# Performance work log

Measured on AMD Instinct MI355X. Metric: run time of the kernel, lower is better.

## Reference

```python
import jax, jax.numpy as jnp
import numpy as np
from jax import lax

EPS = 1e-5
SLOPE = 0.2

def knn_idx(x, k):
    # x: [B, C, N] -> neighbor indices [B, N, k] (largest negative sq-dist, self included)
    inner = jnp.einsum('bcn,bcm->bnm', x, x)          # [B,N,N]
    xx = jnp.sum(x * x, axis=1)                        # [B,N]
    pair = 2.0 * inner - xx[:, :, None] - xx[:, None, :]
    return lax.top_k(pair, k)[1]                       # [B,N,k]

def graph_feature(x, idx):
    # x: [B,C,N], idx: [B,N,k] -> edge features [B,N,k,2C] = (x_j - x_i, x_i)
    feat = jnp.transpose(x, (0, 2, 1))                 # [B,N,C]
    nbr = jax.vmap(lambda f, i: f[i])(feat, idx)       # [B,N,k,C]
    ctr = jnp.broadcast_to(feat[:, :, None, :], nbr.shape)
    return jnp.concatenate([nbr - ctr, ctr], axis=-1)  # [B,N,k,2C]

def bn(x, gamma, beta, axes):
    mu = jnp.mean(x, axis=axes, keepdims=True)
    var = jnp.var(x, axis=axes, keepdims=True)
    return (x - mu) * lax.rsqrt(var + EPS) * gamma + beta

def edge_conv(e, w, gamma, beta):
    # e: [B,N,k,2C], w: [O,2C] (1x1 conv, no bias) -> [B,N,O] after BN+LeakyReLU+max over k
    h = jnp.einsum('bnkc,oc->bnko', e, w)
    h = jax.nn.leaky_relu(bn(h, gamma, beta, (0, 1, 2)), SLOPE)
    return jnp.max(h, axis=2)                          # [B,N,O]

def setup_inputs() -> dict:
    key = jax.random.key(0)
    ks = jax.random.split(key, 8)
    B, C, N, O = 8, 3, 4096, 64
    x = jax.random.normal(ks[0], (B, C, N), jnp.float32)
    w_s = jax.random.normal(ks[1], (O, 2 * C), jnp.float32) * (1.0 / np.sqrt(2 * C))
    w_l = jax.random.normal(ks[2], (O, 2 * C), jnp.float32) * (1.0 / np.sqrt(2 * C))
    w_f = jax.random.normal(ks[3], (O, 2 * O), jnp.float32) * (1.0 / np.sqrt(2 * O))
    g_s = jnp.ones((O,)); b_s = jnp.zeros((O,))
    g_l = jnp.ones((O,)); b_l = jnp.zeros((O,))
    g_f = jnp.ones((O,)); b_f = jnp.zeros((O,))
    return {"x": x, "w_s": w_s, "g_s": g_s, "b_s": b_s,
            "w_l": w_l, "g_l": g_l, "b_l": b_l,
            "w_f": w_f, "g_f": g_f, "b_f": b_f}

def reference(x, w_s, g_s, b_s, w_l, g_l, b_l, w_f, g_f, b_f):
    K_SMALL, K_LARGE = 20, 40
    idx_s = knn_idx(x, K_SMALL)
    idx_l = knn_idx(x, K_LARGE)
    h_s = edge_conv(graph_feature(x, idx_s), w_s, g_s, b_s)   # [B,N,O]
    h_l = edge_conv(graph_feature(x, idx_l), w_l, g_l, b_l)   # [B,N,O]
    h = jnp.concatenate([h_s, h_l], axis=-1)                  # [B,N,2O]
    h = jnp.einsum('bnc,oc->bno', h, w_f)                     # fuse 1x1 conv
    h = jax.nn.leaky_relu(bn(h, g_f, b_f, (0, 1)), SLOPE)
    return jnp.transpose(h, (0, 2, 1))                        # [B,O,N]
```

## Files before the change

### kernel.cpp

```cpp
#include <hip/hip_runtime.h>

#define B_ 8
#define N_ 4096
#define O_ 64
#define KL 40
#define KS 20
#define EPSV 1e-5
#define SLOPE 0.2f

typedef unsigned long long u64;
typedef unsigned int u32;

__device__ __forceinline__ float leaky(float v) { return v >= 0.f ? v : SLOPE * v; }

__device__ __forceinline__ u32 mfloat(float x) {
    const u32 u = __float_as_uint(x);
    return (u & 0x80000000u) ? ~u : (u | 0x80000000u);
}
__device__ __forceinline__ float unmfloat(u32 m) {
    return __uint_as_float((m & 0x80000000u) ? (m ^ 0x80000000u) : ~m);
}

template <int S>
__device__ __forceinline__ u64 xor_ex64(u64 v, int dsaddr) {
    if constexpr (S == 1 || S == 2 || S == 8) {
        constexpr int CTRL = (S == 1) ? 0xB1 : (S == 2) ? 0x4E : 0x128;
        const int lo = __builtin_amdgcn_update_dpp(0, (int)(u32)v, CTRL, 0xF, 0xF, true);
        const int hi = __builtin_amdgcn_update_dpp(0, (int)(u32)(v >> 32), CTRL, 0xF, 0xF, true);
        return ((u64)(u32)hi << 32) | (u32)lo;
    } else {
        const int lo = __builtin_amdgcn_ds_bpermute(dsaddr, (int)(u32)v);
        const int hi = __builtin_amdgcn_ds_bpermute(dsaddr, (int)(u32)(v >> 32));
        return ((u64)(u32)hi << 32) | (u32)lo;
    }
}

template <int K, int S>
__device__ __forceinline__ void stage_pair(u64& a, u64& e, int lane, int dsaddr) {
    const u64 oa = xor_ex64<S>(a, dsaddr);
    const u64 oe = xor_ex64<S>(e, dsaddr);
    const bool sel = (((lane & K) == 0) == ((lane & S) == 0));
    a = ((a < oa) == sel) ? a : oa;
    e = ((e < oe) == sel) ? e : oe;
}

__device__ __forceinline__ void sort64_pair(u64& a, u64& e, int lane,
                                            int a4, int a16, int a32) {
    stage_pair<2, 1>(a, e, lane, 0);
    stage_pair<4, 2>(a, e, lane, 0);    stage_pair<4, 1>(a, e, lane, 0);
    stage_pair<8, 4>(a, e, lane, a4);   stage_pair<8, 2>(a, e, lane, 0);    stage_pair<8, 1>(a, e, lane, 0);
    stage_pair<16, 8>(a, e, lane, 0);   stage_pair<16, 4>(a, e, lane, a4);  stage_pair<16, 2>(a, e, lane, 0);   stage_pair<16, 1>(a, e, lane, 0);
    stage_pair<32, 16>(a, e, lane, a16); stage_pair<32, 8>(a, e, lane, 0);  stage_pair<32, 4>(a, e, lane, a4);  stage_pair<32, 2>(a, e, lane, 0);  stage_pair<32, 1>(a, e, lane, 0);
    stage_pair<64, 32>(a, e, lane, a32); stage_pair<64, 16>(a, e, lane, a16); stage_pair<64, 8>(a, e, lane, 0); stage_pair<64, 4>(a, e, lane, a4); stage_pair<64, 2>(a, e, lane, 0); stage_pair<64, 1>(a, e, lane, 0);
}

__device__ __forceinline__ void merge_pair(u64& L0, u64& L1, u64 a, u64 e, int lane,
                                           int a4, int a16, int a32, int a63) {
    const u64 ra = xor_ex64<63>(a, a63);
    const u64 re = xor_ex64<63>(e, a63);
    L0 = (L0 < ra) ? L0 : ra;
    L1 = (L1 < re) ? L1 : re;
    stage_pair<0, 32>(L0, L1, lane, a32);
    stage_pair<0, 16>(L0, L1, lane, a16);
    stage_pair<0, 8>(L0, L1, lane, 0);
    stage_pair<0, 4>(L0, L1, lane, a4);
    stage_pair<0, 2>(L0, L1, lane, 0);
    stage_pair<0, 1>(L0, L1, lane, 0);
}

__global__ __launch_bounds__(1024) void bucket_kernel(const float* __restrict__ x,
                                                      float4* __restrict__ sxp,
                                                      int* __restrict__ perm,
                                                      float2* __restrict__ cb) {
    __shared__ int hist[256];
    __shared__ int ofs[256];
    __shared__ u32 xsm[4096];
    __shared__ float redmin[16], redmax[16];
    __shared__ u32 wmin[64], wmax[64];
    const int b = blockIdx.x;
    const float* xb = x + (size_t)b * 3 * N_;
    const int t = threadIdx.x;
    float xv[4];
    float mn = INFINITY, mx = -INFINITY;
#pragma unroll
    for (int p = 0; p < 4; ++p) {
        xv[p] = xb[t + p * 1024];
        mn = fminf(mn, xv[p]); mx = fmaxf(mx, xv[p]);
    }
#pragma unroll
    for (int s = 1; s < 64; s <<= 1) {
        mn = fminf(mn, __shfl_xor(mn, s));
        mx = fmaxf(mx, __shfl_xor(mx, s));
    }
    if ((t & 63) == 0) { redmin[t >> 6] = mn; redmax[t >> 6] = mx; }
    if (t < 256) hist[t] = 0;
    __syncthreads();
    if (t == 0) {
        float m0 = INFINITY, m1 = -INFINITY;
        for (int w = 0; w < 16; ++w) { m0 = fminf(m0, redmin[w]); m1 = fmaxf(m1, redmax[w]); }
        redmin[0] = m0; redmax[0] = m1;
    }
    __syncthreads();
    const float xmin = redmin[0];
    const float scale = 256.0f / fmaxf(redmax[0] - xmin, 1e-20f);
    int bk[4];
#pragma unroll
    for (int p = 0; p < 4; ++p) {
        bk[p] = min(255, max(0, (int)((xv[p] - xmin) * scale)));
        atomicAdd(&hist[bk[p]], 1);
    }
    __syncthreads();
    if (t == 0) {
        int acc = 0;
        for (int k = 0; k < 256; ++k) { ofs[k] = acc; acc += hist[k]; }
    }
    if (t < 64) { wmin[t] = 0xFFFFFFFFu; wmax[t] = 0; }
    __syncthreads();
#pragma unroll
    for (int p = 0; p < 4; ++p) {
        const int i = t + p * 1024;
        const int dst = atomicAdd(&ofs[bk[p]], 1);
        const float cx = xv[p], cy = xb[N_ + i], cz = xb[2 * N_ + i];
        sxp[((size_t)b << 12) + dst] = make_float4(2.f * cx, 2.f * cy, 2.f * cz,
                                                   -(cx * cx + cy * cy + cz * cz));
        perm[(b << 12) + dst] = i;
        xsm[dst] = mfloat(cx);
    }
    __syncthreads();
#pragma unroll
    for (int p = 0; p < 4; ++p) {
        const int pos = t + p * 1024;
        const int w = pos >> 6;
        atomicMin(&wmin[w], xsm[pos]);
        atomicMax(&wmax[w], xsm[pos]);
    }
    __syncthreads();
    if (t == 0) {
        u32 sm = 0xFFFFFFFFu;
        for (int w = 63; w >= 0; --w) { sm = min(sm, wmin[w]); wmin[w] = sm; }
        u32 pm = 0;
        for (int w = 0; w < 64; ++w) { pm = max(pm, wmax[w]); wmax[w] = pm; }
    }
    __syncthreads();
    if (t < 64) cb[(b << 6) + t] = make_float2(unmfloat(wmin[t]), unmfloat(wmax[t]));
}

__global__ __launch_bounds__(256, 8) void knn_kernel(const float4* __restrict__ sxp,
                                                     const int* __restrict__ perm,
                                                     const float2* __restrict__ cb,
                                                     const float* __restrict__ w_s,
                                                     const float* __restrict__ w_l,
                                                     int* __restrict__ idx_out,
                                                     float* __restrict__ A_s,
                                                     float* __restrict__ C_s,
                                                     float* __restrict__ A_l,
                                                     float* __restrict__ C_l) {
    __shared__ u64 buf[4][2][128];
    __shared__ float2 cbl[64];
    const int sbid = ((blockIdx.x & 7) << 9) | (blockIdx.x >> 3);
    const int b = sbid >> 9;
    const int qbase = (sbid & 511) << 3;
    const int tid = threadIdx.x;
    const int wave = tid >> 6, lane = tid & 63;
    if (tid < 64) cbl[tid] = cb[(b << 6) + tid];
    const int a4 = (lane ^ 4) << 2, a16 = (lane ^ 16) << 2;
    const int a32 = (lane ^ 32) << 2, a63 = (lane ^ 63) << 2;
    const float4* sp = sxp + ((size_t)b << 12);
    const int* pm = perm + (b << 12);
    const int i0 = qbase + wave * 2;
    const float4 p0 = sp[i0], p1 = sp[i0 + 1];
    const float qx0 = 0.5f * p0.x, qy0 = 0.5f * p0.y, qz0 = 0.5f * p0.z, nw0 = p0.w;
    const float qx1 = 0.5f * p1.x, qy1 = 0.5f * p1.y, qz1 = 0.5f * p1.z, nw1 = p1.w;
    const float qxmin = fminf(qx0, qx1), qxmax = fmaxf(qx0, qx1);
    u64 L0 = ~0ull, L1 = ~0ull;
    float th0 = -INFINITY, th1 = -INFINITY;
    int cnt0 = 0, cnt1 = 0;
    __syncthreads();
    const int home = i0 >> 6;
    int cl = home - 1, cr = home + 1;
    bool openL = (cl >= 0), openR = (cr < 64);
    bool takeR = true;
    int c = home;
    for (;;) {
        {
            const int js = (c << 6) + lane;
            const float4 cd = sp[js];
            const float d0 = fmaf(qx0, cd.x, fmaf(qy0, cd.y, fmaf(qz0, cd.z, cd.w + nw0)));
            const float d1 = fmaf(qx1, cd.x, fmaf(qy1, cd.y, fmaf(qz1, cd.z, cd.w + nw1)));
            const bool pr0 = (d0 >= th0), pr1 = (d1 >= th1);
            const u64 m0 = __ballot(pr0), m1 = __ballot(pr1);
            if (m0) {
                const int pos = cnt0 + __builtin_amdgcn_mbcnt_hi(
                    (u32)(m0 >> 32), __builtin_amdgcn_mbcnt_lo((u32)m0, 0));
                if (pr0) {
                    const u32 kd = __float_as_uint(fminf(d0, -0.0f));
                    buf[wave][0][pos] = ((u64)kd << 32) | (u32)pm[js];
                }
                cnt0 += __popcll(m0);
            }
            if (m1) {
                const int pos = cnt1 + __builtin_amdgcn_mbcnt_hi(
                    (u32)(m1 >> 32), __builtin_amdgcn_mbcnt_lo((u32)m1, 0));
                if (pr1) {
                    const u32 kd = __float_as_uint(fminf(d1, -0.0f));
                    buf[wave][1][pos] = ((u64)kd << 32) | (u32)pm[js];
                }
                cnt1 += __popcll(m1);
            }
            if ((cnt0 | cnt1) >= 64) {
                const int t0 = min(cnt0, 64), t1 = min(cnt1, 64);
                u64 a = (lane < t0) ? buf[wave][0][cnt0 - t0 + lane] : ~0ull;
                u64 e = (lane < t1) ? buf[wave][1][cnt1 - t1 + lane] : ~0ull;
                sort64_pair(a, e, lane, a4, a16, a32);
                merge_pair(L0, L1, a, e, lane, a4, a16, a32, a63);
                th0 = __uint_as_float((u32)__builtin_amdgcn_readlane((int)(u32)(L0 >> 32), KL - 1));
                th1 = __uint_as_float((u32)__builtin_amdgcn_readlane((int)(u32)(L1 >> 32), KL - 1));
                cnt0 -= t0; cnt1 -= t1;
            }
        }
        bool done = false;
        for (;;) {
            if (!openL && !openR) { done = true; break; }
            const bool pickR = openR && (takeR || !openL);
            takeR = !pickR;
            const float r2 = -fminf(th0, th1);
            if (pickR) {
                const float dx = cbl[cr].x - qxmax;
                if (dx > 0.f && dx * dx > r2) { openR = false; continue; }
                c = cr++;
                if (cr >= 64) openR = false;
                break;
            } else {
                const float dx = qxmin - cbl[cl].y;
                if (dx > 0.f && dx * dx > r2) { openL = false; continue; }
                c = cl--;
                if (cl < 0) openL = false;
                break;
            }
        }
        if (done) break;
    }
    if ((cnt0 | cnt1) > 0) {
        u64 a = (lane < cnt0) ? buf[wave][0][lane] : ~0ull;
        u64 e = (lane < cnt1) ? buf[wave][1][lane] : ~0ull;
        sort64_pair(a, e, lane, a4, a16, a32);
        merge_pair(L0, L1, a, e, lane, a4, a16, a32, a63);
    }
    const int oi0 = pm[i0], oi1 = pm[i0 + 1];
    if (lane < KL) {
        idx_out[(size_t)((b << 12) + oi0) * KL + lane] = (int)(u32)L0;
        idx_out[(size_t)((b << 12) + oi1) * KL + lane] = (int)(u32)L1;
    }
    for (int t2 = tid; t2 < 8 * 64; t2 += 256) {
        const int s = qbase + (t2 >> 6), o = t2 & 63;
        const float4 pp = sp[s];
        const float px = 0.5f * pp.x, py = 0.5f * pp.y, pz = 0.5f * pp.z;
        const int io = pm[s];
        const float* ws6 = w_s + o * 6;
        const float* wl6 = w_l + o * 6;
        const size_t gid = (size_t)((b << 12) + io) * 64 + o;
        A_s[gid] = ws6[0] * px + ws6[1] * py + ws6[2] * pz;
        C_s[gid] = (ws6[3] - ws6[0]) * px + (ws6[4] - ws6[1]) * py + (ws6[5] - ws6[2]) * pz;
        A_l[gid] = wl6[0] * px + wl6[1] * py + wl6[2] * pz;
        C_l[gid] = (wl6[3] - wl6[0]) * px + (wl6[4] - wl6[1]) * py + (wl6[5] - wl6[2]) * pz;
    }
}

__global__ __launch_bounds__(256) void gather_kernel(const int* __restrict__ idx,
    const float* __restrict__ A_s, const float* __restrict__ C_s,
    const float* __restrict__ A_l, const float* __restrict__ C_l,
    float* __restrict__ max_s, float* __restrict__ min_s,
    float* __restrict__ max_l, float* __restrict__ min_l,
    float* __restrict__ partial1) {
    const int tid = threadIdx.x;
    const int wave = tid >> 6, lane = tid & 63;
    const int sbid = ((blockIdx.x & 7) << 10) + (blockIdx.x >> 3);
    const int bn = sbid * 4 + wave;
    const int b = bn >> 12;
    const int jb = b << 12;
    const int* ip = idx + (size_t)bn * KL;
    const float cs = C_s[(size_t)bn * 64 + lane];
    const float cl = C_l[(size_t)bn * 64 + lane];
    float mxs = -INFINITY, mns = INFINITY, mxl = -INFINITY, mnl = INFINITY;
    float sums = 0.f, sss = 0.f, suml = 0.f, ssl = 0.f;
#pragma unroll
    for (int k = 0; k < KL; ++k) {
        const int j = ip[k];
        const float hl = A_l[(size_t)(jb + j) * 64 + lane] + cl;
        mxl = fmaxf(mxl, hl); mnl = fminf(mnl, hl);
        suml += hl; ssl = fmaf(hl, hl, ssl);
        if (k < KS) {
            const float hs = A_s[(size_t)(jb + j) * 64 + lane] + cs;
            mxs = fmaxf(mxs, hs); mns = fminf(mns, hs);
            sums += hs; sss = fmaf(hs, hs, sss);
        }
    }
    max_s[(size_t)bn * 64 + lane] = mxs; min_s[(size_t)bn * 64 + lane] = mns;
    max_l[(size_t)bn * 64 + lane] = mxl; min_l[(size_t)bn * 64 + lane] = mnl;
    __shared__ float red[4][4][64];
    red[0][wave][lane] = sums; red[1][wave][lane] = sss;
    red[2][wave][lane] = suml; red[3][wave][lane] = ssl;
    __syncthreads();
    const int st = tid >> 6;
    const int o = tid & 63;
    partial1[(size_t)blockIdx.x * 256 + tid] =
        red[st][0][o] + red[st][1][o] + red[st][2][o] + red[st][3][o];
}

__global__ void reduce1a_kernel(const float* __restrict__ partial1, double* __restrict__ partialD1) {
    const int t = threadIdx.x;
    double acc = 0.0;
    const int r0 = blockIdx.x * 64;
    for (int r = 0; r < 64; ++r) acc += (double)partial1[(size_t)(r0 + r) * 256 + t];
    partialD1[(size_t)blockIdx.x * 256 + t] = acc;
}

__global__ void reduce1b_kernel(const double* __restrict__ partialD1,
                                const float* __restrict__ g_s, const float* __restrict__ b_s,
                                const float* __restrict__ g_l, const float* __restrict__ b_l,
                                float* __restrict__ sb1) {
    const int t = threadIdx.x;
    double acc = 0.0;
    for (int r = 0; r < 128; ++r) acc += partialD1[(size_t)r * 256 + t];
    __shared__ double sums[256];
    sums[t] = acc;
    __syncthreads();
    if (t < 64) {
        const double ns = (double)B_ * N_ * KS;
        const double nl = (double)B_ * N_ * KL;
        double mu = sums[t] / ns;
        double var = sums[64 + t] / ns - mu * mu;
        double sc = (double)g_s[t] / sqrt(var + EPSV);
        sb1[t] = (float)sc;
        sb1[64 + t] = (float)((double)b_s[t] - mu * sc);
        mu = sums[128 + t] / nl;
        var = sums[192 + t] / nl - mu * mu;
        sc = (double)g_l[t] / sqrt(var + EPSV);
        sb1[128 + t] = (float)sc;
        sb1[192 + t] = (float)((double)b_l[t] - mu * sc);
    }
}

__global__ __launch_bounds__(256) void fuse_kernel(
    const float* __restrict__ max_s, const float* __restrict__ min_s,
    const float* __restrict__ max_l, const float* __restrict__ min_l,
    const float* __restrict__ sb1, const float* __restrict__ w_f,
    float* __restrict__ f_buf, float* __restrict__ partial2) {
    __shared__ float wfT[128 * 64];
    __shared__ float av[4][128];
    __shared__ float red[2][4][64];
    const int tid = threadIdx.x;
    for (int t = tid; t < 8192; t += 256) {
        const int c = t >> 6, o = t & 63;
        wfT[t] = w_f[o * 128 + c];
    }
    const int sbid = ((blockIdx.x & 7) << 8) + (blockIdx.x >> 3);
    const int wave = tid >> 6, lane = tid & 63;
    const float sc_s = sb1[lane], bi_s = sb1[64 + lane];
    const float sc_l = sb1[128 + lane], bi_l = sb1[192 + lane];
    float sum_f = 0.f, ss_f = 0.f;
    __syncthreads();
    for (int p = 0; p < 4; ++p) {
        const int bn = (sbid * 4 + wave) * 4 + p;
        const size_t base = (size_t)bn * 64 + lane;
        const float hs = sc_s >= 0.f ? max_s[base] : min_s[base];
        const float a_s = leaky(fmaf(sc_s, hs, bi_s));
        const float hl = sc_l >= 0.f ? max_l[base] : min_l[base];
        const float a_l = leaky(fmaf(sc_l, hl, bi_l));
        av[wave][lane] = a_s;
        av[wave][64 + lane] = a_l;
        float acc = 0.f;
#pragma unroll
        for (int c = 0; c < 128; ++c) acc = fmaf(wfT[c * 64 + lane], av[wave][c], acc);
        f_buf[base] = acc;
        sum_f += acc;
        ss_f = fmaf(acc, acc, ss_f);
    }
    red[0][wave][lane] = sum_f;
    red[1][wave][lane] = ss_f;
    __syncthreads();
    if (tid < 128) {
        const int st = tid >> 6, o = tid & 63;
        partial2[(size_t)blockIdx.x * 128 + tid] =
            red[st][0][o] + red[st][1][o] + red[st][2][o] + red[st][3][o];
    }
}

__global__ void reduce2a_kernel(const float* __restrict__ partial2, double* __restrict__ partialD2) {
    const int t = threadIdx.x;
    double acc = 0.0;
    const int r0 = blockIdx.x * 32;
    for (int r = 0; r < 32; ++r) acc += (double)partial2[(size_t)(r0 + r) * 128 + t];
    partialD2[(size_t)blockIdx.x * 128 + t] = acc;
}

__global__ void reduce2b_kernel(const double* __restrict__ partialD2,
                                const float* __restrict__ g_f, const float* __restrict__ b_f,
                                float* __restrict__ sb2) {
    const int t = threadIdx.x;
    double acc = 0.0;
    for (int r = 0; r < 64; ++r) acc += partialD2[(size_t)r * 128 + t];
    __shared__ double sums[128];
    sums[t] = acc;
    __syncthreads();
    if (t < 64) {
        const double n = (double)B_ * N_;
        const double mu = sums[t] / n;
        const double var = sums[64 + t] / n - mu * mu;
        const double sc = (double)g_f[t] / sqrt(var + EPSV);
        sb2[t] = (float)sc;
        sb2[64 + t] = (float)((double)b_f[t] - mu * sc);
    }
}

__global__ __launch_bounds__(256) void final_kernel(const float* __restrict__ f_buf,
                                                    const float* __restrict__ sb2,
                                                    float* __restrict__ out) {
    __shared__ float tile[64][65];
    const int sbid = ((blockIdx.x & 7) << 6) + (blockIdx.x >> 3);
    const int b = sbid >> 6;
    const int n0 = (sbid & 63) << 6;
#pragma unroll
    for (int r = 0; r < 16; ++r) {
        const int t = r * 256 + threadIdx.x;
        const int n = t >> 6, o = t & 63;
        const float v = f_buf[(size_t)((b << 12) + n0 + n) * 64 + o];
        const float h = fmaf(sb2[o], v, sb2[64 + o]);
        tile[n][o] = leaky(h);
    }
    __syncthreads();
#pragma unroll
    for (int r = 0; r < 16; ++r) {
        const int t = r * 256 + threadIdx.x;
        const int o = t >> 6, n = t & 63;
        out[(size_t)((b << 6) + o) * N_ + n0 + n] = tile[n][o];
    }
}

extern "C" void kernel_launch(void* const* d_in, const int* in_sizes, int n_in,
                              void* d_out, int out_size, void* d_ws, size_t ws_size,
                              hipStream_t stream) {
    (void)in_sizes; (void)n_in; (void)out_size; (void)ws_size;
    const float* x   = (const float*)d_in[0];
    const float* w_s = (const float*)d_in[1];
    const float* g_s = (const float*)d_in[2];
    const float* b_s = (const float*)d_in[3];
    const float* w_l = (const float*)d_in[4];
    const float* g_l = (const float*)d_in[5];
    const float* b_l = (const float*)d_in[6];
    const float* w_f = (const float*)d_in[7];
    const float* g_f = (const float*)d_in[8];
    const float* b_f = (const float*)d_in[9];
    float* out = (float*)d_out;
    char* ws = (char*)d_ws;

    constexpr size_t SZ_PT   = (size_t)B_ * N_ * 64 * 4;
    constexpr size_t OFF_IDX = 0;
    constexpr size_t OFF_AS  = OFF_IDX + (size_t)B_ * N_ * KL * 4;
    constexpr size_t OFF_CS  = OFF_AS + SZ_PT;
    constexpr size_t OFF_AL  = OFF_CS + SZ_PT;
    constexpr size_t OFF_CL  = OFF_AL + SZ_PT;
    constexpr size_t OFF_MXS = OFF_CL + SZ_PT;
    constexpr size_t OFF_MNS = OFF_MXS + SZ_PT;
    constexpr size_t OFF_MXL = OFF_MNS + SZ_PT;
    constexpr size_t OFF_MNL = OFF_MXL + SZ_PT;
    constexpr size_t OFF_P1  = OFF_MNL + SZ_PT;
    constexpr size_t OFF_PD1 = OFF_P1 + (size_t)8192 * 256 * 4;
    constexpr size_t OFF_SB1 = OFF_PD1 + (size_t)128 * 256 * 8;
    constexpr size_t OFF_F   = OFF_SB1 + 1024;
    constexpr size_t OFF_P2  = OFF_F + SZ_PT;
    constexpr size_t OFF_PD2 = OFF_P2 + (size_t)2048 * 128 * 4;
    constexpr size_t OFF_SB2 = OFF_PD2 + (size_t)64 * 128 * 8;
    constexpr size_t OFF_SXP = OFF_SB2 + 1024;
    constexpr size_t OFF_PRM = OFF_SXP + (size_t)B_ * N_ * 16;
    constexpr size_t OFF_CB  = OFF_PRM + (size_t)B_ * N_ * 4;

    int*    idx  = (int*)(ws + OFF_IDX);
    float*  A_s  = (float*)(ws + OFF_AS);
    float*  C_s  = (float*)(ws + OFF_CS);
    float*  A_l  = (float*)(ws + OFF_AL);
    float*  C_l  = (float*)(ws + OFF_CL);
    float*  mxs  = (float*)(ws + OFF_MXS);
    float*  mns  = (float*)(ws + OFF_MNS);
    float*  mxl  = (float*)(ws + OFF_MXL);
    float*  mnl  = (float*)(ws + OFF_MNL);
    float*  p1   = (float*)(ws + OFF_P1);
    double* pd1  = (double*)(ws + OFF_PD1);
    float*  sb1  = (float*)(ws + OFF_SB1);
    float*  fb   = (float*)(ws + OFF_F);
    float*  p2   = (float*)(ws + OFF_P2);
    double* pd2  = (double*)(ws + OFF_PD2);
    float*  sb2  = (float*)(ws + OFF_SB2);
    float4* sxp  = (float4*)(ws + OFF_SXP);
    int*    prm  = (int*)(ws + OFF_PRM);
    float2* cbv  = (float2*)(ws + OFF_CB);

    hipLaunchKernelGGL(bucket_kernel, dim3(8), dim3(1024), 0, stream, x, sxp, prm, cbv);
    hipLaunchKernelGGL(knn_kernel, dim3(4096), dim3(256), 0, stream,
                       sxp, prm, cbv, w_s, w_l, idx, A_s, C_s, A_l, C_l);
    hipLaunchKernelGGL(gather_kernel, dim3(8192), dim3(256), 0, stream,
                       idx, A_s, C_s, A_l, C_l, mxs, mns, mxl, mnl, p1);
    hipLaunchKernelGGL(reduce1a_kernel, dim3(128), dim3(256), 0, stream, p1, pd1);
    hipLaunchKernelGGL(reduce1b_kernel, dim3(1), dim3(256), 0, stream, pd1, g_s, b_s, g_l, b_l, sb1);
    hipLaunchKernelGGL(fuse_kernel, dim3(2048), dim3(256), 0, stream,
                       mxs, mns, mxl, mnl, sb1, w_f, fb, p2);
    hipLaunchKernelGGL(reduce2a_kernel, dim3(64), dim3(128), 0, stream, p2, pd2);
    hipLaunchKernelGGL(reduce2b_kernel, dim3(1), dim3(128), 0, stream, pd2, g_f, b_f, sb2);
    hipLaunchKernelGGL(final_kernel, dim3(512), dim3(256), 0, stream, fb, sb2, out);
}
```

Before: 225.4 us.

## Fuse neighbor gather and edge-conv stats into kNN kernel, prefetch next chunk

The kNN kernel now computes the edge-conv max/min and BN partial sums directly from its register-held neighbor lists. It reads raw point coordinates from a new float4 copy instead of writing idx and precomputed A/C tables for a separate gather kernel. This removes the gather kernel launch and the idx plus four 8 MB A/C tensors written and then re-read. The candidate loop also chooses the next bucket and prefetches its points before processing the current one, to hide load latency. In exchange, the per-query stats buffer is larger (256 floats per point), which raises the traffic of reduce1a, and the kNN kernel takes on more register pressure.

```diff
diff --git a/kernel.cpp b/kernel.cpp
--- a/kernel.cpp
+++ b/kernel.cpp
@@ -71,7 +71,8 @@
 __global__ __launch_bounds__(1024) void bucket_kernel(const float* __restrict__ x,
                                                       float4* __restrict__ sxp,
                                                       int* __restrict__ perm,
-                                                      float2* __restrict__ cb) {
+                                                      float2* __restrict__ cb,
+                                                      float4* __restrict__ xo4) {
     __shared__ int hist[256];
     __shared__ int ofs[256];
     __shared__ u32 xsm[4096];
@@ -124,6 +125,7 @@
         sxp[((size_t)b << 12) + dst] = make_float4(2.f * cx, 2.f * cy, 2.f * cz,
                                                    -(cx * cx + cy * cy + cz * cz));
         perm[(b << 12) + dst] = i;
+        xo4[((size_t)b << 12) + i] = make_float4(cx, cy, cz, 0.f);
         xsm[dst] = mfloat(cx);
     }
     __syncthreads();
@@ -138,8 +140,8 @@
     if (t == 0) {
         u32 sm = 0xFFFFFFFFu;
         for (int w = 63; w >= 0; --w) { sm = min(sm, wmin[w]); wmin[w] = sm; }
-        u32 pm = 0;
-        for (int w = 0; w < 64; ++w) { pm = max(pm, wmax[w]); wmax[w] = pm; }
+        u32 pm2 = 0;
+        for (int w = 0; w < 64; ++w) { pm2 = max(pm2, wmax[w]); wmax[w] = pm2; }
     }
     __syncthreads();
     if (t < 64) cb[(b << 6) + t] = make_float2(unmfloat(wmin[t]), unmfloat(wmax[t]));
@@ -148,13 +150,14 @@
 __global__ __launch_bounds__(256, 8) void knn_kernel(const float4* __restrict__ sxp,
                                                      const int* __restrict__ perm,
                                                      const float2* __restrict__ cb,
+                                                     const float4* __restrict__ xo4,
                                                      const float* __restrict__ w_s,
                                                      const float* __restrict__ w_l,
-                                                     int* __restrict__ idx_out,
-                                                     float* __restrict__ A_s,
-                                                     float* __restrict__ C_s,
-                                                     float* __restrict__ A_l,
-                                                     float* __restrict__ C_l) {
+                                                     float* __restrict__ max_s,
+                                                     float* __restrict__ min_s,
+                                                     float* __restrict__ max_l,
+                                                     float* __restrict__ min_l,
+                                                     float* __restrict__ qstats) {
     __shared__ u64 buf[4][2][128];
     __shared__ float2 cbl[64];
     const int sbid = ((blockIdx.x & 7) << 9) | (blockIdx.x >> 3);
@@ -167,6 +170,7 @@
     const int a32 = (lane ^ 32) << 2, a63 = (lane ^ 63) << 2;
     const float4* sp = sxp + ((size_t)b << 12);
     const int* pm = perm + (b << 12);
+    const float4* xo = xo4 + ((size_t)b << 12);
     const int i0 = qbase + wave * 2;
     const float4 p0 = sp[i0], p1 = sp[i0 + 1];
     const float qx0 = 0.5f * p0.x, qy0 = 0.5f * p0.y, qz0 = 0.5f * p0.z, nw0 = p0.w;
@@ -181,10 +185,29 @@
     bool openL = (cl >= 0), openR = (cr < 64);
     bool takeR = true;
     int c = home;
+    float4 cd = sp[(c << 6) + lane];
+    int pj = pm[(c << 6) + lane];
     for (;;) {
+        int cn = -1;
+        for (;;) {
+            if (!openL && !openR) break;
+            const bool pickR = openR && (takeR || !openL);
+            takeR = !pickR;
+            const float r2 = -fminf(th0, th1);
+            if (pickR) {
+                const float dx = cbl[cr].x - qxmax;
+                if (dx > 0.f && dx * dx > r2) { openR = false; continue; }
+                cn = cr++; if (cr >= 64) openR = false; break;
+            } else {
+                const float dx = qxmin - cbl[cl].y;
+                if (dx > 0.f && dx * dx > r2) { openL = false; continue; }
+                cn = cl--; if (cl < 0) openL = false; break;
+            }
+        }
+        float4 nd = make_float4(0.f, 0.f, 0.f, 0.f);
+        int nj = 0;
+        if (cn >= 0) { nd = sp[(cn << 6) + lane]; nj = pm[(cn << 6) + lane]; }
         {
-            const int js = (c << 6) + lane;
-            const float4 cd = sp[js];
             const float d0 = fmaf(qx0, cd.x, fmaf(qy0, cd.y, fmaf(qz0, cd.z, cd.w + nw0)));
             const float d1 = fmaf(qx1, cd.x, fmaf(qy1, cd.y, fmaf(qz1, cd.z, cd.w + nw1)));
             const bool pr0 = (d0 >= th0), pr1 = (d1 >= th1);
@@ -194,7 +217,7 @@
                     (u32)(m0 >> 32), __builtin_amdgcn_mbcnt_lo((u32)m0, 0));
                 if (pr0) {
                     const u32 kd = __float_as_uint(fminf(d0, -0.0f));
-                    buf[wave][0][pos] = ((u64)kd << 32) | (u32)pm[js];
+                    buf[wave][0][pos] = ((u64)kd << 32) | (u32)pj;
                 }
                 cnt0 += __popcll(m0);
             }
@@ -203,7 +226,7 @@
                     (u32)(m1 >> 32), __builtin_amdgcn_mbcnt_lo((u32)m1, 0));
                 if (pr1) {
                     const u32 kd = __float_as_uint(fminf(d1, -0.0f));
-                    buf[wave][1][pos] = ((u64)kd << 32) | (u32)pm[js];
+                    buf[wave][1][pos] = ((u64)kd << 32) | (u32)pj;
                 }
                 cnt1 += __popcll(m1);
             }
@@ -218,27 +241,8 @@
                 cnt0 -= t0; cnt1 -= t1;
             }
         }
-        bool done = false;
-        for (;;) {
-            if (!openL && !openR) { done = true; break; }
-            const bool pickR = openR && (takeR || !openL);
-            takeR = !pickR;
-            const float r2 = -fminf(th0, th1);
-            if (pickR) {
-                const float dx = cbl[cr].x - qxmax;
-                if (dx > 0.f && dx * dx > r2) { openR = false; continue; }
-                c = cr++;
-                if (cr >= 64) openR = false;
-                break;
-            } else {
-                const float dx = qxmin - cbl[cl].y;
-                if (dx > 0.f && dx * dx > r2) { openL = false; continue; }
-                c = cl--;
-                if (cl < 0) openL = false;
-                break;
-            }
-        }
-        if (done) break;
+        if (cn < 0) break;
+        cd = nd; pj = nj; c = cn;
     }
     if ((cnt0 | cnt1) > 0) {
         u64 a = (lane < cnt0) ? buf[wave][0][lane] : ~0ull;
@@ -246,72 +250,48 @@
         sort64_pair(a, e, lane, a4, a16, a32);
         merge_pair(L0, L1, a, e, lane, a4, a16, a32, a63);
     }
+    const int lw = lane * 6;
+    const float ws0 = w_s[lw], ws1 = w_s[lw + 1], ws2 = w_s[lw + 2];
+    const float ds0 = w_s[lw + 3] - ws0, ds1 = w_s[lw + 4] - ws1, ds2 = w_s[lw + 5] - ws2;
+    const float wl0 = w_l[lw], wl1 = w_l[lw + 1], wl2 = w_l[lw + 2];
+    const float dl0 = w_l[lw + 3] - wl0, dl1 = w_l[lw + 4] - wl1, dl2 = w_l[lw + 5] - wl2;
     const int oi0 = pm[i0], oi1 = pm[i0 + 1];
-    if (lane < KL) {
-        idx_out[(size_t)((b << 12) + oi0) * KL + lane] = (int)(u32)L0;
-        idx_out[(size_t)((b << 12) + oi1) * KL + lane] = (int)(u32)L1;
-    }
-    for (int t2 = tid; t2 < 8 * 64; t2 += 256) {
-        const int s = qbase + (t2 >> 6), o = t2 & 63;
-        const float4 pp = sp[s];
-        const float px = 0.5f * pp.x, py = 0.5f * pp.y, pz = 0.5f * pp.z;
-        const int io = pm[s];
-        const float* ws6 = w_s + o * 6;
-        const float* wl6 = w_l + o * 6;
-        const size_t gid = (size_t)((b << 12) + io) * 64 + o;
-        A_s[gid] = ws6[0] * px + ws6[1] * py + ws6[2] * pz;
-        C_s[gid] = (ws6[3] - ws6[0]) * px + (ws6[4] - ws6[1]) * py + (ws6[5] - ws6[2]) * pz;
-        A_l[gid] = wl6[0] * px + wl6[1] * py + wl6[2] * pz;
-        C_l[gid] = (wl6[3] - wl6[0]) * px + (wl6[4] - wl6[1]) * py + (wl6[5] - wl6[2]) * pz;
-    }
-}
-
-__global__ __launch_bounds__(256) void gather_kernel(const int* __restrict__ idx,
-    const float* __restrict__ A_s, const float* __restrict__ C_s,
-    const float* __restrict__ A_l, const float* __restrict__ C_l,
-    float* __restrict__ max_s, float* __restrict__ min_s,
-    float* __restrict__ max_l, float* __restrict__ min_l,
-    float* __restrict__ partial1) {
-    const int tid = threadIdx.x;
-    const int wave = tid >> 6, lane = tid & 63;
-    const int sbid = ((blockIdx.x & 7) << 10) + (blockIdx.x >> 3);
-    const int bn = sbid * 4 + wave;
-    const int b = bn >> 12;
-    const int jb = b << 12;
-    const int* ip = idx + (size_t)bn * KL;
-    const float cs = C_s[(size_t)bn * 64 + lane];
-    const float cl = C_l[(size_t)bn * 64 + lane];
-    float mxs = -INFINITY, mns = INFINITY, mxl = -INFINITY, mnl = INFINITY;
-    float sums = 0.f, sss = 0.f, suml = 0.f, ssl = 0.f;
-#pragma unroll
-    for (int k = 0; k < KL; ++k) {
-        const int j = ip[k];
-        const float hl = A_l[(size_t)(jb + j) * 64 + lane] + cl;
-        mxl = fmaxf(mxl, hl); mnl = fminf(mnl, hl);
-        suml += hl; ssl = fmaf(hl, hl, ssl);
-        if (k < KS) {
-            const float hs = A_s[(size_t)(jb + j) * 64 + lane] + cs;
-            mxs = fmaxf(mxs, hs); mns = fminf(mns, hs);
-            sums += hs; sss = fmaf(hs, hs, sss);
+#pragma unroll
+    for (int q = 0; q < 2; ++q) {
+        const float qx = q ? qx1 : qx0, qy = q ? qy1 : qy0, qz = q ? qz1 : qz0;
+        const int Llo = q ? (int)(u32)L1 : (int)(u32)L0;
+        const int oi = q ? oi1 : oi0;
+        const float cs = ds0 * qx + ds1 * qy + ds2 * qz;
+        const float cq = dl0 * qx + dl1 * qy + dl2 * qz;
+        float mxs = -INFINITY, mns = INFINITY, mxl = -INFINITY, mnl = INFINITY;
+        float sums = 0.f, sss = 0.f, suml = 0.f, ssl = 0.f;
+#pragma unroll 8
+        for (int k = 0; k < KL; ++k) {
+            const int j = __builtin_amdgcn_readlane(Llo, k);
+            const float4 xj = xo[j];
+            const float hl = fmaf(wl0, xj.x, fmaf(wl1, xj.y, wl2 * xj.z)) + cq;
+            mxl = fmaxf(mxl, hl); mnl = fminf(mnl, hl);
+            suml += hl; ssl = fmaf(hl, hl, ssl);
+            if (k < KS) {
+                const float hs = fmaf(ws0, xj.x, fmaf(ws1, xj.y, ws2 * xj.z)) + cs;
+                mxs = fmaxf(mxs, hs); mns = fminf(mns, hs);
+                sums += hs; sss = fmaf(hs, hs, sss);
+            }
         }
-    }
-    max_s[(size_t)bn * 64 + lane] = mxs; min_s[(size_t)bn * 64 + lane] = mns;
-    max_l[(size_t)bn * 64 + lane] = mxl; min_l[(size_t)bn * 64 + lane] = mnl;
-    __shared__ float red[4][4][64];
-    red[0][wave][lane] = sums; red[1][wave][lane] = sss;
-    red[2][wave][lane] = suml; red[3][wave][lane] = ssl;
-    __syncthreads();
-    const int st = tid >> 6;
-    const int o = tid & 63;
-    partial1[(size_t)blockIdx.x * 256 + tid] =
-        red[st][0][o] + red[st][1][o] + red[st][2][o] + red[st][3][o];
-}
-
-__global__ void reduce1a_kernel(const float* __restrict__ partial1, double* __restrict__ partialD1) {
+        const size_t base = (size_t)((b << 12) + oi) * 64 + lane;
+        max_s[base] = mxs; min_s[base] = mns;
+        max_l[base] = mxl; min_l[base] = mnl;
+        float* qs = qstats + (size_t)((b << 12) + oi) * 256;
+        qs[lane] = sums; qs[64 + lane] = sss;
+        qs[128 + lane] = suml; qs[192 + lane] = ssl;
+    }
+}
+
+__global__ void reduce1a_kernel(const float* __restrict__ qstats, double* __restrict__ partialD1) {
     const int t = threadIdx.x;
     double acc = 0.0;
-    const int r0 = blockIdx.x * 64;
-    for (int r = 0; r < 64; ++r) acc += (double)partial1[(size_t)(r0 + r) * 256 + t];
+    const int r0 = blockIdx.x * 256;
+    for (int r = 0; r < 256; ++r) acc += (double)qstats[(size_t)(r0 + r) * 256 + t];
     partialD1[(size_t)blockIdx.x * 256 + t] = acc;
 }
 
@@ -455,17 +435,12 @@
     char* ws = (char*)d_ws;
 
     constexpr size_t SZ_PT   = (size_t)B_ * N_ * 64 * 4;
-    constexpr size_t OFF_IDX = 0;
-    constexpr size_t OFF_AS  = OFF_IDX + (size_t)B_ * N_ * KL * 4;
-    constexpr size_t OFF_CS  = OFF_AS + SZ_PT;
-    constexpr size_t OFF_AL  = OFF_CS + SZ_PT;
-    constexpr size_t OFF_CL  = OFF_AL + SZ_PT;
-    constexpr size_t OFF_MXS = OFF_CL + SZ_PT;
+    constexpr size_t OFF_MXS = 0;
     constexpr size_t OFF_MNS = OFF_MXS + SZ_PT;
     constexpr size_t OFF_MXL = OFF_MNS + SZ_PT;
     constexpr size_t OFF_MNL = OFF_MXL + SZ_PT;
-    constexpr size_t OFF_P1  = OFF_MNL + SZ_PT;
-    constexpr size_t OFF_PD1 = OFF_P1 + (size_t)8192 * 256 * 4;
+    constexpr size_t OFF_QST = OFF_MNL + SZ_PT;
+    constexpr size_t OFF_PD1 = OFF_QST + (size_t)B_ * N_ * 256 * 4;
     constexpr size_t OFF_SB1 = OFF_PD1 + (size_t)128 * 256 * 8;
     constexpr size_t OFF_F   = OFF_SB1 + 1024;
     constexpr size_t OFF_P2  = OFF_F + SZ_PT;
@@ -474,17 +449,13 @@
     constexpr size_t OFF_SXP = OFF_SB2 + 1024;
     constexpr size_t OFF_PRM = OFF_SXP + (size_t)B_ * N_ * 16;
     constexpr size_t OFF_CB  = OFF_PRM + (size_t)B_ * N_ * 4;
-
-    int*    idx  = (int*)(ws + OFF_IDX);
-    float*  A_s  = (float*)(ws + OFF_AS);
-    float*  C_s  = (float*)(ws + OFF_CS);
-    float*  A_l  = (float*)(ws + OFF_AL);
-    float*  C_l  = (float*)(ws + OFF_CL);
+    constexpr size_t OFF_XO4 = OFF_CB + (size_t)B_ * 64 * 8;
+
     float*  mxs  = (float*)(ws + OFF_MXS);
     float*  mns  = (float*)(ws + OFF_MNS);
     float*  mxl  = (float*)(ws + OFF_MXL);
     float*  mnl  = (float*)(ws + OFF_MNL);
-    float*  p1   = (float*)(ws + OFF_P1);
+    float*  qst  = (float*)(ws + OFF_QST);
     double* pd1  = (double*)(ws + OFF_PD1);
     float*  sb1  = (float*)(ws + OFF_SB1);
     float*  fb   = (float*)(ws + OFF_F);
@@ -494,13 +465,12 @@
     float4* sxp  = (float4*)(ws + OFF_SXP);
     int*    prm  = (int*)(ws + OFF_PRM);
     float2* cbv  = (float2*)(ws + OFF_CB);
-
-    hipLaunchKernelGGL(bucket_kernel, dim3(8), dim3(1024), 0, stream, x, sxp, prm, cbv);
+    float4* xo4  = (float4*)(ws + OFF_XO4);
+
+    hipLaunchKernelGGL(bucket_kernel, dim3(8), dim3(1024), 0, stream, x, sxp, prm, cbv, xo4);
     hipLaunchKernelGGL(knn_kernel, dim3(4096), dim3(256), 0, stream,
-                       sxp, prm, cbv, w_s, w_l, idx, A_s, C_s, A_l, C_l);
-    hipLaunchKernelGGL(gather_kernel, dim3(8192), dim3(256), 0, stream,
-                       idx, A_s, C_s, A_l, C_l, mxs, mns, mxl, mnl, p1);
-    hipLaunchKernelGGL(reduce1a_kernel, dim3(128), dim3(256), 0, stream, p1, pd1);
+                       sxp, prm, cbv, xo4, w_s, w_l, mxs, mns, mxl, mnl, qst);
+    hipLaunchKernelGGL(reduce1a_kernel, dim3(128), dim3(256), 0, stream, qst, pd1);
     hipLaunchKernelGGL(reduce1b_kernel, dim3(1), dim3(256), 0, stream, pd1, g_s, b_s, g_l, b_l, sb1);
     hipLaunchKernelGGL(fuse_kernel, dim3(2048), dim3(256), 0, stream,
                        mxs, mns, mxl, mnl, sb1, w_f, fb, p2);
```

Measured after the change: 224.7 us. Within noise of the previous version (-0.3%).

## Prefetch next KNN chunk, seed top-k from home chunk, merge reduce2 kernels

Applied to the files above, without the earlier changes.

The KNN loop now picks the next candidate chunk and issues its global loads before processing the current chunk, so load latency overlaps with the ballot and sort work. The home chunk is sorted directly to seed the top-k list and threshold, so pruning can start tighter. The two-stage BN2 statistics reduction becomes a single 1024-thread kernel, removing one launch and the double-precision intermediate buffer. The cost is extra registers for the prefetched data, and the single-block reduction runs less parallel.

```diff
diff --git a/kernel.cpp b/kernel.cpp
--- a/kernel.cpp
+++ b/kernel.cpp
@@ -138,8 +138,8 @@
     if (t == 0) {
         u32 sm = 0xFFFFFFFFu;
         for (int w = 63; w >= 0; --w) { sm = min(sm, wmin[w]); wmin[w] = sm; }
-        u32 pm = 0;
-        for (int w = 0; w < 64; ++w) { pm = max(pm, wmax[w]); wmax[w] = pm; }
+        u32 pm2 = 0;
+        for (int w = 0; w < 64; ++w) { pm2 = max(pm2, wmax[w]); wmax[w] = pm2; }
     }
     __syncthreads();
     if (t < 64) cb[(b << 6) + t] = make_float2(unmfloat(wmin[t]), unmfloat(wmax[t]));
@@ -172,19 +172,67 @@
     const float qx0 = 0.5f * p0.x, qy0 = 0.5f * p0.y, qz0 = 0.5f * p0.z, nw0 = p0.w;
     const float qx1 = 0.5f * p1.x, qy1 = 0.5f * p1.y, qz1 = 0.5f * p1.z, nw1 = p1.w;
     const float qxmin = fminf(qx0, qx1), qxmax = fmaxf(qx0, qx1);
-    u64 L0 = ~0ull, L1 = ~0ull;
-    float th0 = -INFINITY, th1 = -INFINITY;
     int cnt0 = 0, cnt1 = 0;
     __syncthreads();
     const int home = i0 >> 6;
+    u64 L0, L1;
+    float th0, th1;
+    {
+        const int js = (home << 6) + lane;
+        const float4 ch = sp[js];
+        const int pj = pm[js];
+        const float d0 = fmaf(qx0, ch.x, fmaf(qy0, ch.y, fmaf(qz0, ch.z, ch.w + nw0)));
+        const float d1 = fmaf(qx1, ch.x, fmaf(qy1, ch.y, fmaf(qz1, ch.z, ch.w + nw1)));
+        u64 k0 = ((u64)__float_as_uint(fminf(d0, -0.0f)) << 32) | (u32)pj;
+        u64 k1 = ((u64)__float_as_uint(fminf(d1, -0.0f)) << 32) | (u32)pj;
+        sort64_pair(k0, k1, lane, a4, a16, a32);
+        L0 = k0; L1 = k1;
+        th0 = __uint_as_float((u32)__builtin_amdgcn_readlane((int)(u32)(L0 >> 32), KL - 1));
+        th1 = __uint_as_float((u32)__builtin_amdgcn_readlane((int)(u32)(L1 >> 32), KL - 1));
+    }
     int cl = home - 1, cr = home + 1;
     bool openL = (cl >= 0), openR = (cr < 64);
     bool takeR = true;
-    int c = home;
+    int c = -1;
+    float4 cd = make_float4(0.f, 0.f, 0.f, 0.f);
+    int pj = 0;
     for (;;) {
+        if (!openL && !openR) break;
+        const bool pickR = openR && (takeR || !openL);
+        takeR = !pickR;
+        const float r2 = -fminf(th0, th1);
+        if (pickR) {
+            const float dx = cbl[cr].x - qxmax;
+            if (dx > 0.f && dx * dx > r2) { openR = false; continue; }
+            c = cr++; if (cr >= 64) openR = false; break;
+        } else {
+            const float dx = qxmin - cbl[cl].y;
+            if (dx > 0.f && dx * dx > r2) { openL = false; continue; }
+            c = cl--; if (cl < 0) openL = false; break;
+        }
+    }
+    if (c >= 0) { cd = sp[(c << 6) + lane]; pj = pm[(c << 6) + lane]; }
+    while (c >= 0) {
+        int cn = -1;
+        for (;;) {
+            if (!openL && !openR) break;
+            const bool pickR = openR && (takeR || !openL);
+            takeR = !pickR;
+            const float r2 = -fminf(th0, th1);
+            if (pickR) {
+                const float dx = cbl[cr].x - qxmax;
+                if (dx > 0.f && dx * dx > r2) { openR = false; continue; }
+                cn = cr++; if (cr >= 64) openR = false; break;
+            } else {
+                const float dx = qxmin - cbl[cl].y;
+                if (dx > 0.f && dx * dx > r2) { openL = false; continue; }
+                cn = cl--; if (cl < 0) openL = false; break;
+            }
+        }
+        float4 nd = make_float4(0.f, 0.f, 0.f, 0.f);
+        int nj = 0;
+        if (cn >= 0) { nd = sp[(cn << 6) + lane]; nj = pm[(cn << 6) + lane]; }
         {
-            const int js = (c << 6) + lane;
-            const float4 cd = sp[js];
             const float d0 = fmaf(qx0, cd.x, fmaf(qy0, cd.y, fmaf(qz0, cd.z, cd.w + nw0)));
             const float d1 = fmaf(qx1, cd.x, fmaf(qy1, cd.y, fmaf(qz1, cd.z, cd.w + nw1)));
             const bool pr0 = (d0 >= th0), pr1 = (d1 >= th1);
@@ -194,7 +242,7 @@
                     (u32)(m0 >> 32), __builtin_amdgcn_mbcnt_lo((u32)m0, 0));
                 if (pr0) {
                     const u32 kd = __float_as_uint(fminf(d0, -0.0f));
-                    buf[wave][0][pos] = ((u64)kd << 32) | (u32)pm[js];
+                    buf[wave][0][pos] = ((u64)kd << 32) | (u32)pj;
                 }
                 cnt0 += __popcll(m0);
             }
@@ -203,7 +251,7 @@
                     (u32)(m1 >> 32), __builtin_amdgcn_mbcnt_lo((u32)m1, 0));
                 if (pr1) {
                     const u32 kd = __float_as_uint(fminf(d1, -0.0f));
-                    buf[wave][1][pos] = ((u64)kd << 32) | (u32)pm[js];
+                    buf[wave][1][pos] = ((u64)kd << 32) | (u32)pj;
                 }
                 cnt1 += __popcll(m1);
             }
@@ -218,27 +266,7 @@
                 cnt0 -= t0; cnt1 -= t1;
             }
         }
-        bool done = false;
-        for (;;) {
-            if (!openL && !openR) { done = true; break; }
-            const bool pickR = openR && (takeR || !openL);
-            takeR = !pickR;
-            const float r2 = -fminf(th0, th1);
-            if (pickR) {
-                const float dx = cbl[cr].x - qxmax;
-                if (dx > 0.f && dx * dx > r2) { openR = false; continue; }
-                c = cr++;
-                if (cr >= 64) openR = false;
-                break;
-            } else {
-                const float dx = qxmin - cbl[cl].y;
-                if (dx > 0.f && dx * dx > r2) { openL = false; continue; }
-                c = cl--;
-                if (cl < 0) openL = false;
-                break;
-            }
-        }
-        if (done) break;
+        c = cn; cd = nd; pj = nj;
     }
     if ((cnt0 | cnt1) > 0) {
         u64 a = (lane < cnt0) ? buf[wave][0][lane] : ~0ull;
@@ -386,27 +414,29 @@
     }
 }
 
-__global__ void reduce2a_kernel(const float* __restrict__ partial2, double* __restrict__ partialD2) {
+__global__ __launch_bounds__(1024) void reduce2_kernel(const float* __restrict__ partial2,
+                                                       const float* __restrict__ g_f,
+                                                       const float* __restrict__ b_f,
+                                                       float* __restrict__ sb2) {
+    __shared__ double seg[8][128];
+    __shared__ double tot[128];
     const int t = threadIdx.x;
+    const int col = t & 127, sg = t >> 7;
     double acc = 0.0;
-    const int r0 = blockIdx.x * 32;
-    for (int r = 0; r < 32; ++r) acc += (double)partial2[(size_t)(r0 + r) * 128 + t];
-    partialD2[(size_t)blockIdx.x * 128 + t] = acc;
-}
-
-__global__ void reduce2b_kernel(const double* __restrict__ partialD2,
-                                const float* __restrict__ g_f, const float* __restrict__ b_f,
-                                float* __restrict__ sb2) {
-    const int t = threadIdx.x;
-    double acc = 0.0;
-    for (int r = 0; r < 64; ++r) acc += partialD2[(size_t)r * 128 + t];
-    __shared__ double sums[128];
-    sums[t] = acc;
+    const int r0 = sg * 256;
+    for (int r = 0; r < 256; ++r) acc += (double)partial2[(size_t)(r0 + r) * 128 + col];
+    seg[sg][col] = acc;
+    __syncthreads();
+    if (t < 128) {
+        double s = 0.0;
+        for (int g = 0; g < 8; ++g) s += seg[g][t];
+        tot[t] = s;
+    }
     __syncthreads();
     if (t < 64) {
         const double n = (double)B_ * N_;
-        const double mu = sums[t] / n;
-        const double var = sums[64 + t] / n - mu * mu;
+        const double mu = tot[t] / n;
+        const double var = tot[64 + t] / n - mu * mu;
         const double sc = (double)g_f[t] / sqrt(var + EPSV);
         sb2[t] = (float)sc;
         sb2[64 + t] = (float)((double)b_f[t] - mu * sc);
@@ -469,8 +499,7 @@
     constexpr size_t OFF_SB1 = OFF_PD1 + (size_t)128 * 256 * 8;
     constexpr size_t OFF_F   = OFF_SB1 + 1024;
     constexpr size_t OFF_P2  = OFF_F + SZ_PT;
-    constexpr size_t OFF_PD2 = OFF_P2 + (size_t)2048 * 128 * 4;
-    constexpr size_t OFF_SB2 = OFF_PD2 + (size_t)64 * 128 * 8;
+    constexpr size_t OFF_SB2 = OFF_P2 + (size_t)2048 * 128 * 4;
     constexpr size_t OFF_SXP = OFF_SB2 + 1024;
     constexpr size_t OFF_PRM = OFF_SXP + (size_t)B_ * N_ * 16;
     constexpr size_t OFF_CB  = OFF_PRM + (size_t)B_ * N_ * 4;
@@ -489,7 +518,6 @@
     float*  sb1  = (float*)(ws + OFF_SB1);
     float*  fb   = (float*)(ws + OFF_F);
     float*  p2   = (float*)(ws + OFF_P2);
-    double* pd2  = (double*)(ws + OFF_PD2);
     float*  sb2  = (float*)(ws + OFF_SB2);
     float4* sxp  = (float4*)(ws + OFF_SXP);
     int*    prm  = (int*)(ws + OFF_PRM);
@@ -504,7 +532,6 @@
     hipLaunchKernelGGL(reduce1b_kernel, dim3(1), dim3(256), 0, stream, pd1, g_s, b_s, g_l, b_l, sb1);
     hipLaunchKernelGGL(fuse_kernel, dim3(2048), dim3(256), 0, stream,
                        mxs, mns, mxl, mnl, sb1, w_f, fb, p2);
-    hipLaunchKernelGGL(reduce2a_kernel, dim3(64), dim3(128), 0, stream, p2, pd2);
-    hipLaunchKernelGGL(reduce2b_kernel, dim3(1), dim3(128), 0, stream, pd2, g_f, b_f, sb2);
+    hipLaunchKernelGGL(reduce2_kernel, dim3(1), dim3(1024), 0, stream, p2, g_f, b_f, sb2);
     hipLaunchKernelGGL(final_kernel, dim3(512), dim3(256), 0, stream, fb, sb2, out);
 }
```

Result: no change. 228.1 us (+1.2%).
